# Optimization experiments

Hardware: AMD Instinct MI355X
Metric: run time of the kernel (lower is better)

Reference implementation:

```python
import jax, jax.numpy as jnp
import numpy as np

B, S, E, A, DK, H = 8, 2048, 256, 16, 64, 64  # batch, seq, embed, action, d_key, mlp hidden


def setup_inputs() -> dict:
    key = jax.random.key(0)
    ks = jax.random.split(key, 8)
    obs = jax.random.normal(ks[0], (B, S, E), dtype=jnp.float32)
    act = jnp.zeros((B, S, A), dtype=jnp.float32)  # one-hot actions; unused by forward
    # projection weights stored as [in, out] (torch Linear applies x @ W.T)
    Wq = jax.random.normal(ks[1], (E, DK), dtype=jnp.float32) / np.sqrt(E)
    Wk = jax.random.normal(ks[2], (E, DK), dtype=jnp.float32) / np.sqrt(E)
    Wv = jax.random.normal(ks[3], (E, DK), dtype=jnp.float32) / np.sqrt(E)
    W1 = jax.random.normal(ks[4], (DK, H), dtype=jnp.float32) / np.sqrt(DK)
    b1 = jnp.zeros((H,), dtype=jnp.float32)
    W2 = jax.random.normal(ks[5], (H, 1), dtype=jnp.float32) / np.sqrt(H)
    b2 = jnp.zeros((1,), dtype=jnp.float32)
    return dict(obs=obs, act=act, Wq=Wq, Wk=Wk, Wv=Wv, W1=W1, b1=b1, W2=W2, b2=b2)


def reference(obs, act, Wq, Wk, Wv, W1, b1, W2, b2):
    b, s, _ = obs.shape
    dk = Wq.shape[1]
    scale = dk ** -0.25  # applied to both q and k, net 1/sqrt(dk)
    q = (obs @ Wq) * scale          # [b, s, dk]
    k = (obs @ Wk) * scale          # [b, s, dk]
    v = obs @ Wv                    # [b, s, dk]
    scores = jnp.einsum('bqd,bkd->bqk', q, k)  # [b, s, s]
    causal = jnp.tril(jnp.ones((s, s), dtype=bool))
    scores = jnp.where(causal[None], scores, -jnp.inf)
    attn = jax.nn.softmax(scores, axis=2)      # [b, s, s]
    attn_out = jnp.einsum('bqk,bkd->bqd', attn, v)  # [b, s, dk]
    h = jax.nn.relu(attn_out.reshape(b * s, dk) @ W1 + b1)
    x = h @ W2 + b2                 # [b*s, 1]
    return (x, attn)
```

## Files before the change

### kernel.cpp

```cpp
#include <hip/hip_runtime.h>
#include <hip/hip_bf16.h>
#include <math.h>

#define NB 8
#define SQ 2048
#define NSP 8

typedef __attribute__((ext_vector_type(8))) short short8;
typedef __attribute__((ext_vector_type(4))) float f32x4;

__device__ __forceinline__ short f2bf(float f) {
    union { float f; unsigned u; } v; v.f = f;
    unsigned r = v.u + 0x7FFF + ((v.u >> 16) & 1);
    return (short)(r >> 16);
}
__device__ __forceinline__ float bf2f(short s) {
    union { unsigned u; float f; } v; v.u = ((unsigned)(unsigned short)s) << 16;
    return v.f;
}

__global__ __launch_bounds__(256) void k_wt(const float* __restrict__ Wq,
                                            const float* __restrict__ Wk,
                                            const float* __restrict__ Wv,
                                            short* __restrict__ wt) {
    int o = blockIdx.x * 256 + threadIdx.x;
    int row = o >> 8, e = o & 255;
    int w = row >> 6, d = row & 63;
    const float* W = (w == 0) ? Wq : ((w == 1) ? Wk : Wv);
    wt[o] = f2bf(W[e * 64 + d]);
}

__global__ __launch_bounds__(256, 4) void k_proj(const float* __restrict__ obs,
                                                 const short* __restrict__ wt,
                                                 short* __restrict__ qw,
                                                 short* __restrict__ kw,
                                                 short* __restrict__ vt) {
    int tid = threadIdx.x, w = tid >> 6, l = tid & 63, lg = l >> 4, lc = l & 15;
    int r0 = blockIdx.x * 16;
    int arow = r0 + lc;
    f32x4 accq = {0.f,0.f,0.f,0.f}, acck = {0.f,0.f,0.f,0.f}, accv = {0.f,0.f,0.f,0.f};
    const short* wq = wt + (size_t)(w * 16 + lc) * 256;
    const short* wk = wt + (size_t)(64 + w * 16 + lc) * 256;
    const short* wv = wt + (size_t)(128 + w * 16 + lc) * 256;
    #pragma unroll
    for (int ks = 0; ks < 8; ++ks) {
        int e0 = ks * 32 + lg * 8;
        const float* ap = obs + (size_t)arow * 256 + e0;
        float4 f0 = *(const float4*)ap;
        float4 f1 = *(const float4*)(ap + 4);
        short8 a;
        a[0] = f2bf(f0.x); a[1] = f2bf(f0.y); a[2] = f2bf(f0.z); a[3] = f2bf(f0.w);
        a[4] = f2bf(f1.x); a[5] = f2bf(f1.y); a[6] = f2bf(f1.z); a[7] = f2bf(f1.w);
        accq = __builtin_amdgcn_mfma_f32_16x16x32_bf16(a, *(const short8*)(wq + e0), accq, 0, 0, 0);
        acck = __builtin_amdgcn_mfma_f32_16x16x32_bf16(a, *(const short8*)(wk + e0), acck, 0, 0, 0);
        accv = __builtin_amdgcn_mfma_f32_16x16x32_bf16(a, *(const short8*)(wv + e0), accv, 0, 0, 0);
    }
    const float scale = 0.35355339059327373f;
    __shared__ short ldsv[64][18];
    #pragma unroll
    for (int r = 0; r < 4; ++r) {
        int row = r0 + lg * 4 + r;
        qw[(size_t)row * 64 + w * 16 + lc] = f2bf(accq[r] * scale);
        kw[(size_t)row * 64 + w * 16 + lc] = f2bf(acck[r] * scale);
        ldsv[w * 16 + lc][lg * 4 + r] = f2bf(accv[r]);
    }
    __syncthreads();
    int b = r0 >> 11, s0 = r0 & 2047;
    int d = tid >> 2, sc = (tid & 3) * 4;
    short* dst = vt + (size_t)b * 64 * SQ + (size_t)d * SQ + s0 + sc;
    dst[0] = ldsv[d][sc]; dst[1] = ldsv[d][sc + 1];
    dst[2] = ldsv[d][sc + 2]; dst[3] = ldsv[d][sc + 3];
}

__global__ __launch_bounds__(256) void k_flash(const short* __restrict__ qw,
                                               const short* __restrict__ kw,
                                               const short* __restrict__ vt,
                                               float* __restrict__ op,
                                               float* __restrict__ lpart,
                                               short* __restrict__ pbuf) {
    int qb = blockIdx.x, sp = blockIdx.y, b = blockIdx.z;
    if (sp > qb) return;
    int q0 = qb * 64;
    int tid = threadIdx.x, w = tid >> 6, l = tid & 63, lg = l >> 4, lc = l & 15;
    int r0 = q0 + w * 16;
    int eo = lg * 8;
    __shared__ short ldsP[4][16][72];
    const short* qbase = qw + (size_t)b * SQ * 64;
    const short* kbase = kw + (size_t)b * SQ * 64;
    const short* vbase = vt + (size_t)b * 64 * SQ;
    short* pbase = pbuf + (size_t)b * SQ * SQ;
    short8 qf0 = *(const short8*)(qbase + (size_t)(r0 + lc) * 64 + eo);
    short8 qf1 = *(const short8*)(qbase + (size_t)(r0 + lc) * 64 + 32 + eo);
    float lsum[4];
    f32x4 o[4];
    #pragma unroll
    for (int r = 0; r < 4; ++r) lsum[r] = 0.f;
    #pragma unroll
    for (int nj = 0; nj < 4; ++nj) o[nj] = (f32x4){0.f, 0.f, 0.f, 0.f};

    for (int kb = sp; kb <= qb; kb += NSP) {
        int k0 = kb * 64;
        f32x4 s[4];
        #pragma unroll
        for (int nj = 0; nj < 4; ++nj) s[nj] = (f32x4){0.f, 0.f, 0.f, 0.f};
        #pragma unroll
        for (int nj = 0; nj < 4; ++nj) {
            short8 kf = *(const short8*)(kbase + (size_t)(k0 + nj * 16 + lc) * 64 + eo);
            s[nj] = __builtin_amdgcn_mfma_f32_16x16x32_bf16(qf0, kf, s[nj], 0, 0, 0);
        }
        #pragma unroll
        for (int nj = 0; nj < 4; ++nj) {
            short8 kf = *(const short8*)(kbase + (size_t)(k0 + nj * 16 + lc) * 64 + 32 + eo);
            s[nj] = __builtin_amdgcn_mfma_f32_16x16x32_bf16(qf1, kf, s[nj], 0, 0, 0);
        }
        if (kb == qb) {
            #pragma unroll
            for (int nj = 0; nj < 4; ++nj)
                #pragma unroll
                for (int r = 0; r < 4; ++r)
                    if (k0 + nj * 16 + lc > r0 + lg * 4 + r) s[nj][r] = -INFINITY;
        }
        #pragma unroll
        for (int r = 0; r < 4; ++r) {
            float ps = 0.f;
            #pragma unroll
            for (int nj = 0; nj < 4; ++nj) {
                float p = __expf(s[nj][r]);
                ps += p;
                ldsP[w][lg * 4 + r][nj * 16 + lc] = f2bf(p);
            }
            ps += __shfl_xor(ps, 1);
            ps += __shfl_xor(ps, 2);
            ps += __shfl_xor(ps, 4);
            ps += __shfl_xor(ps, 8);
            lsum[r] += ps;
        }
        #pragma unroll
        for (int ks = 0; ks < 2; ++ks) {
            short8 pa = *(const short8*)&ldsP[w][lc][ks * 32 + lg * 8];
            *(short8*)(pbase + (size_t)(r0 + lc) * SQ + k0 + ks * 32 + lg * 8) = pa;
            #pragma unroll
            for (int nj = 0; nj < 4; ++nj) {
                short8 vf = *(const short8*)(vbase + (size_t)(nj * 16 + lc) * SQ + k0 + ks * 32 + eo);
                o[nj] = __builtin_amdgcn_mfma_f32_16x16x32_bf16(pa, vf, o[nj], 0, 0, 0);
            }
        }
    }
    size_t pb = ((size_t)sp * NB + b) * SQ;
    #pragma unroll
    for (int r = 0; r < 4; ++r) {
        int row = r0 + lg * 4 + r;
        if (lc == 0) lpart[pb + row] = lsum[r];
        #pragma unroll
        for (int nj = 0; nj < 4; ++nj)
            op[(pb + row) * 64 + nj * 16 + lc] = o[nj][r];
    }
}

__global__ __launch_bounds__(256) void k_combine(const float* __restrict__ op,
                                                 const float* __restrict__ lpart,
                                                 const float* __restrict__ W1,
                                                 const float* __restrict__ b1,
                                                 const float* __restrict__ W2,
                                                 const float* __restrict__ b2,
                                                 float* __restrict__ x,
                                                 float* __restrict__ linv) {
    int row0 = blockIdx.x * 8;
    int tid = threadIdx.x, w = tid >> 6, l = tid & 63;
    __shared__ float w1l[64][64];
    __shared__ float aol[8][64];
    {
        const float4* src = (const float4*)W1;
        float4* dst = (float4*)&w1l[0][0];
        #pragma unroll
        for (int i = 0; i < 4; ++i) dst[tid + i * 256] = src[tid + i * 256];
    }
    #pragma unroll
    for (int rr = 0; rr < 2; ++rr) {
        int grow = row0 + w * 2 + rr;
        int b = grow >> 11, s = grow & 2047;
        int nsp = (s >> 6) + 1; if (nsp > NSP) nsp = NSP;
        float od = 0.f, lt = 0.f;
        for (int sp = 0; sp < nsp; ++sp) {
            size_t base = (size_t)(sp * NB + b) * SQ + s;
            od += op[base * 64 + l];
            lt += lpart[base];
        }
        float inv = 1.f / lt;
        aol[w * 2 + rr][l] = od * inv;
        if (l == 0) linv[grow] = inv;
    }
    __syncthreads();
    #pragma unroll
    for (int rr = 0; rr < 2; ++rr) {
        int grow = row0 + w * 2 + rr;
        float t = b1[l];
        #pragma unroll 16
        for (int d = 0; d < 64; ++d) t += aol[w * 2 + rr][d] * w1l[d][l];
        float h = fmaxf(t, 0.f);
        float px = h * W2[l];
        px += __shfl_xor(px, 1);
        px += __shfl_xor(px, 2);
        px += __shfl_xor(px, 4);
        px += __shfl_xor(px, 8);
        px += __shfl_xor(px, 16);
        px += __shfl_xor(px, 32);
        if (l == 0) x[grow] = px + b2[0];
    }
}

__global__ __launch_bounds__(256) void k_write(const short* __restrict__ pbuf,
                                               const float* __restrict__ linv,
                                               float* __restrict__ attn) {
    int csp = blockIdx.x, qb = blockIdx.y, b = blockIdx.z;
    int tid = threadIdx.x, w = tid >> 6, l = tid & 63;
    __shared__ float liv[64];
    if (tid < 64) liv[tid] = linv[(size_t)b * SQ + qb * 64 + tid];
    __syncthreads();
    float* abase = attn + (size_t)b * SQ * SQ;
    int colb = csp * 256 + l * 4;
    if ((colb >> 6) > qb) {
        float4 z = {0.f, 0.f, 0.f, 0.f};
        #pragma unroll
        for (int r = 0; r < 16; ++r) {
            int row = qb * 64 + w * 16 + r;
            *(float4*)(abase + (size_t)row * SQ + colb) = z;
        }
        return;
    }
    const short* pbase = pbuf + (size_t)b * SQ * SQ;
    #pragma unroll
    for (int r = 0; r < 16; ++r) {
        int row = qb * 64 + w * 16 + r;
        float inv = liv[w * 16 + r];
        short4 pv = *(const short4*)(pbase + (size_t)row * SQ + colb);
        float4 o;
        o.x = bf2f(pv.x) * inv;
        o.y = bf2f(pv.y) * inv;
        o.z = bf2f(pv.z) * inv;
        o.w = bf2f(pv.w) * inv;
        *(float4*)(abase + (size_t)row * SQ + colb) = o;
    }
}

extern "C" void kernel_launch(void* const* d_in, const int* in_sizes, int n_in,
                              void* d_out, int out_size, void* d_ws, size_t ws_size,
                              hipStream_t stream) {
    const float* obs = (const float*)d_in[0];
    const float* Wq  = (const float*)d_in[2];
    const float* Wk  = (const float*)d_in[3];
    const float* Wv  = (const float*)d_in[4];
    const float* W1  = (const float*)d_in[5];
    const float* b1  = (const float*)d_in[6];
    const float* W2  = (const float*)d_in[7];
    const float* b2  = (const float*)d_in[8];

    float* x    = (float*)d_out;
    float* attn = (float*)d_out + NB * SQ;

    float* op = attn;

    char* ws = (char*)d_ws;
    short* wt    = (short*)(ws);
    short* qw    = (short*)(ws + 131072);
    short* kw    = (short*)(ws + 2228224);
    short* vt    = (short*)(ws + 4325376);
    float* lpart = (float*)(ws + 6422528);
    float* linv  = (float*)(ws + 6946816);
    short* pbuf  = (short*)(ws + 7012352);

    k_wt<<<dim3(192), dim3(256), 0, stream>>>(Wq, Wk, Wv, wt);
    k_proj<<<dim3(1024), dim3(256), 0, stream>>>(obs, wt, qw, kw, vt);
    k_flash<<<dim3(32, NSP, NB), dim3(256), 0, stream>>>(qw, kw, vt, op, lpart, pbuf);
    k_combine<<<dim3(2048), dim3(256), 0, stream>>>(op, lpart, W1, b1, W2, b2, x, linv);
    k_write<<<dim3(8, 32, NB), dim3(256), 0, stream>>>(pbuf, linv, attn);
}
```

Baseline: 143.0 us.

## Fuse all stages into one cooperative persistent kernel with grid syncs

Replaces the five separate launches (weight transpose, projection, flash attention, combine, attn write) with a single cooperative persistent kernel. Each stage loops over work items by block index and is separated from the next by grid.sync(), so per-launch gaps and tail effects are removed. The row-sum of softmax probabilities is now taken with an MFMA against a vector of bf16 ones instead of shuffle reductions, which sums the bf16-rounded values rather than the fp32 ones. Grid barriers and the smaller grid size (set from occupancy) may cost load balance compared with separate launches, and the original launch path is kept as a fallback.

Measured after the change: 355.3 us. 148% more time.

```diff
diff --git a/kernel.cpp b/kernel.cpp
--- a/kernel.cpp
+++ b/kernel.cpp
@@ -1,5 +1,6 @@
 #include <hip/hip_runtime.h>
 #include <hip/hip_bf16.h>
+#include <hip/hip_cooperative_groups.h>
 #include <math.h>
 
 #define NB 8
@@ -17,6 +18,226 @@
 __device__ __forceinline__ float bf2f(short s) {
     union { unsigned u; float f; } v; v.u = ((unsigned)(unsigned short)s) << 16;
     return v.f;
+}
+
+__global__ __launch_bounds__(256, 4) void k_mega(
+    const float* __restrict__ obs, const float* __restrict__ Wq,
+    const float* __restrict__ Wk,  const float* __restrict__ Wv,
+    const float* __restrict__ W1,  const float* __restrict__ b1,
+    const float* __restrict__ W2,  const float* __restrict__ b2,
+    float* __restrict__ x, float* __restrict__ attn,
+    short* __restrict__ wt, short* __restrict__ qw, short* __restrict__ kw,
+    short* __restrict__ vt, float* __restrict__ lpart, float* __restrict__ linv,
+    short* __restrict__ pbuf, float* __restrict__ op)
+{
+    namespace cg = cooperative_groups;
+    cg::grid_group grid = cg::this_grid();
+    __shared__ __align__(16) char smem[18688];
+    const int bid = threadIdx.y * 0 + blockIdx.x;
+    const int tid = threadIdx.x, w = tid >> 6, l = tid & 63, lg = l >> 4, lc = l & 15;
+    const int gsz = gridDim.x;
+    short8 ones;
+    #pragma unroll
+    for (int i = 0; i < 8; ++i) ones[i] = (short)0x3F80;
+
+    for (int o = bid * 256 + tid; o < 192 * 256; o += gsz * 256) {
+        int row = o >> 8, e = o & 255;
+        int wsel = row >> 6, d = row & 63;
+        const float* W = (wsel == 0) ? Wq : ((wsel == 1) ? Wk : Wv);
+        wt[o] = f2bf(W[e * 64 + d]);
+    }
+    grid.sync();
+
+    {
+        short (*ldsv)[18] = (short(*)[18])smem;
+        for (int tb = bid; tb < 1024; tb += gsz) {
+            int r0 = tb * 16;
+            int arow = r0 + lc;
+            f32x4 accq = {0.f,0.f,0.f,0.f}, acck = {0.f,0.f,0.f,0.f}, accv = {0.f,0.f,0.f,0.f};
+            const short* wqp = wt + (size_t)(w * 16 + lc) * 256;
+            const short* wkp = wt + (size_t)(64 + w * 16 + lc) * 256;
+            const short* wvp = wt + (size_t)(128 + w * 16 + lc) * 256;
+            #pragma unroll
+            for (int ks = 0; ks < 8; ++ks) {
+                int e0 = ks * 32 + lg * 8;
+                const float* ap = obs + (size_t)arow * 256 + e0;
+                float4 f0 = *(const float4*)ap;
+                float4 f1 = *(const float4*)(ap + 4);
+                short8 a;
+                a[0] = f2bf(f0.x); a[1] = f2bf(f0.y); a[2] = f2bf(f0.z); a[3] = f2bf(f0.w);
+                a[4] = f2bf(f1.x); a[5] = f2bf(f1.y); a[6] = f2bf(f1.z); a[7] = f2bf(f1.w);
+                accq = __builtin_amdgcn_mfma_f32_16x16x32_bf16(a, *(const short8*)(wqp + e0), accq, 0, 0, 0);
+                acck = __builtin_amdgcn_mfma_f32_16x16x32_bf16(a, *(const short8*)(wkp + e0), acck, 0, 0, 0);
+                accv = __builtin_amdgcn_mfma_f32_16x16x32_bf16(a, *(const short8*)(wvp + e0), accv, 0, 0, 0);
+            }
+            const float scale = 0.35355339059327373f;
+            #pragma unroll
+            for (int r = 0; r < 4; ++r) {
+                int row = r0 + lg * 4 + r;
+                qw[(size_t)row * 64 + w * 16 + lc] = f2bf(accq[r] * scale);
+                kw[(size_t)row * 64 + w * 16 + lc] = f2bf(acck[r] * scale);
+                ldsv[w * 16 + lc][lg * 4 + r] = f2bf(accv[r]);
+            }
+            __syncthreads();
+            int b = r0 >> 11, s0 = r0 & 2047;
+            int d = tid >> 2, sc = (tid & 3) * 4;
+            short* dst = vt + (size_t)b * 64 * SQ + (size_t)d * SQ + s0 + sc;
+            dst[0] = ldsv[d][sc]; dst[1] = ldsv[d][sc + 1];
+            dst[2] = ldsv[d][sc + 2]; dst[3] = ldsv[d][sc + 3];
+            __syncthreads();
+        }
+    }
+    grid.sync();
+
+    {
+        short (*ldsP)[16][72] = (short(*)[16][72])smem;
+        for (int vb = bid; vb < 32 * NSP * NB; vb += gsz) {
+            int qb = vb & 31, sp = (vb >> 5) & 7, b = vb >> 8;
+            if (sp > qb) continue;
+            int q0 = qb * 64;
+            int r0 = q0 + w * 16;
+            int eo = lg * 8;
+            const short* qbase = qw + (size_t)b * SQ * 64;
+            const short* kbase = kw + (size_t)b * SQ * 64;
+            const short* vbase = vt + (size_t)b * 64 * SQ;
+            short* pbase = pbuf + (size_t)b * SQ * SQ;
+            short8 qf0 = *(const short8*)(qbase + (size_t)(r0 + lc) * 64 + eo);
+            short8 qf1 = *(const short8*)(qbase + (size_t)(r0 + lc) * 64 + 32 + eo);
+            f32x4 osum = {0.f, 0.f, 0.f, 0.f};
+            f32x4 o[4];
+            #pragma unroll
+            for (int nj = 0; nj < 4; ++nj) o[nj] = (f32x4){0.f, 0.f, 0.f, 0.f};
+
+            for (int kb = sp; kb <= qb; kb += NSP) {
+                int k0 = kb * 64;
+                f32x4 s[4];
+                #pragma unroll
+                for (int nj = 0; nj < 4; ++nj) s[nj] = (f32x4){0.f, 0.f, 0.f, 0.f};
+                #pragma unroll
+                for (int nj = 0; nj < 4; ++nj) {
+                    short8 kf = *(const short8*)(kbase + (size_t)(k0 + nj * 16 + lc) * 64 + eo);
+                    s[nj] = __builtin_amdgcn_mfma_f32_16x16x32_bf16(qf0, kf, s[nj], 0, 0, 0);
+                }
+                #pragma unroll
+                for (int nj = 0; nj < 4; ++nj) {
+                    short8 kf = *(const short8*)(kbase + (size_t)(k0 + nj * 16 + lc) * 64 + 32 + eo);
+                    s[nj] = __builtin_amdgcn_mfma_f32_16x16x32_bf16(qf1, kf, s[nj], 0, 0, 0);
+                }
+                if (kb == qb) {
+                    #pragma unroll
+                    for (int nj = 0; nj < 4; ++nj)
+                        #pragma unroll
+                        for (int r = 0; r < 4; ++r)
+                            if (k0 + nj * 16 + lc > r0 + lg * 4 + r) s[nj][r] = -INFINITY;
+                }
+                #pragma unroll
+                for (int r = 0; r < 4; ++r)
+                    #pragma unroll
+                    for (int nj = 0; nj < 4; ++nj)
+                        ldsP[w][lg * 4 + r][nj * 16 + lc] = f2bf(__expf(s[nj][r]));
+                #pragma unroll
+                for (int ks = 0; ks < 2; ++ks) {
+                    short8 pa = *(const short8*)&ldsP[w][lc][ks * 32 + lg * 8];
+                    *(short8*)(pbase + (size_t)(r0 + lc) * SQ + k0 + ks * 32 + lg * 8) = pa;
+                    osum = __builtin_amdgcn_mfma_f32_16x16x32_bf16(pa, ones, osum, 0, 0, 0);
+                    #pragma unroll
+                    for (int nj = 0; nj < 4; ++nj) {
+                        short8 vf = *(const short8*)(vbase + (size_t)(nj * 16 + lc) * SQ + k0 + ks * 32 + eo);
+                        o[nj] = __builtin_amdgcn_mfma_f32_16x16x32_bf16(pa, vf, o[nj], 0, 0, 0);
+                    }
+                }
+            }
+            size_t pb = ((size_t)sp * NB + b) * SQ;
+            #pragma unroll
+            for (int r = 0; r < 4; ++r) {
+                int row = r0 + lg * 4 + r;
+                if (lc == 0) lpart[pb + row] = osum[r];
+                #pragma unroll
+                for (int nj = 0; nj < 4; ++nj)
+                    op[(pb + row) * 64 + nj * 16 + lc] = o[nj][r];
+            }
+        }
+    }
+    grid.sync();
+
+    {
+        float* w1l = (float*)smem;
+        float (*aol)[64] = (float(*)[64])(smem + 16384);
+        const float4* src = (const float4*)W1;
+        float4* dst = (float4*)w1l;
+        #pragma unroll
+        for (int i = 0; i < 4; ++i) dst[tid + i * 256] = src[tid + i * 256];
+        __syncthreads();
+        for (int vb = bid; vb < 2048; vb += gsz) {
+            int row0 = vb * 8;
+            #pragma unroll
+            for (int rr = 0; rr < 2; ++rr) {
+                int grow = row0 + w * 2 + rr;
+                int b = grow >> 11, s = grow & 2047;
+                int nsp = (s >> 6) + 1; if (nsp > NSP) nsp = NSP;
+                float od = 0.f, lt = 0.f;
+                for (int sp = 0; sp < nsp; ++sp) {
+                    size_t base = (size_t)(sp * NB + b) * SQ + s;
+                    od += op[base * 64 + l];
+                    lt += lpart[base];
+                }
+                float inv = 1.f / lt;
+                aol[w * 2 + rr][l] = od * inv;
+                if (l == 0) linv[grow] = inv;
+            }
+            #pragma unroll
+            for (int rr = 0; rr < 2; ++rr) {
+                int grow = row0 + w * 2 + rr;
+                float t = b1[l];
+                #pragma unroll 16
+                for (int d = 0; d < 64; ++d) t += aol[w * 2 + rr][d] * w1l[d * 64 + l];
+                float h = fmaxf(t, 0.f);
+                float px = h * W2[l];
+                px += __shfl_xor(px, 1);
+                px += __shfl_xor(px, 2);
+                px += __shfl_xor(px, 4);
+                px += __shfl_xor(px, 8);
+                px += __shfl_xor(px, 16);
+                px += __shfl_xor(px, 32);
+                if (l == 0) x[grow] = px + b2[0];
+            }
+        }
+    }
+    grid.sync();
+
+    {
+        float* liv = (float*)smem;
+        for (int vb = bid; vb < 2048; vb += gsz) {
+            int csp = vb & 7, qb = (vb >> 3) & 31, b = vb >> 8;
+            __syncthreads();
+            if (tid < 64) liv[tid] = linv[(size_t)b * SQ + qb * 64 + tid];
+            __syncthreads();
+            float* abase = attn + (size_t)b * SQ * SQ;
+            int colb = csp * 256 + l * 4;
+            if ((colb >> 6) > qb) {
+                float4 z = {0.f, 0.f, 0.f, 0.f};
+                #pragma unroll
+                for (int r = 0; r < 16; ++r) {
+                    int row = qb * 64 + w * 16 + r;
+                    *(float4*)(abase + (size_t)row * SQ + colb) = z;
+                }
+            } else {
+                const short* pbase = pbuf + (size_t)b * SQ * SQ;
+                #pragma unroll
+                for (int r = 0; r < 16; ++r) {
+                    int row = qb * 64 + w * 16 + r;
+                    float inv = liv[w * 16 + r];
+                    short4 pv = *(const short4*)(pbase + (size_t)row * SQ + colb);
+                    float4 o;
+                    o.x = bf2f(pv.x) * inv;
+                    o.y = bf2f(pv.y) * inv;
+                    o.z = bf2f(pv.z) * inv;
+                    o.w = bf2f(pv.w) * inv;
+                    *(float4*)(abase + (size_t)row * SQ + colb) = o;
+                }
+            }
+        }
+    }
 }
 
 __global__ __launch_bounds__(256) void k_wt(const float* __restrict__ Wq,
@@ -91,10 +312,11 @@
     short* pbase = pbuf + (size_t)b * SQ * SQ;
     short8 qf0 = *(const short8*)(qbase + (size_t)(r0 + lc) * 64 + eo);
     short8 qf1 = *(const short8*)(qbase + (size_t)(r0 + lc) * 64 + 32 + eo);
-    float lsum[4];
+    short8 ones;
+    #pragma unroll
+    for (int i = 0; i < 8; ++i) ones[i] = (short)0x3F80;
+    f32x4 osum = {0.f, 0.f, 0.f, 0.f};
     f32x4 o[4];
-    #pragma unroll
-    for (int r = 0; r < 4; ++r) lsum[r] = 0.f;
     #pragma unroll
     for (int nj = 0; nj < 4; ++nj) o[nj] = (f32x4){0.f, 0.f, 0.f, 0.f};
 
@@ -121,24 +343,15 @@
                     if (k0 + nj * 16 + lc > r0 + lg * 4 + r) s[nj][r] = -INFINITY;
         }
         #pragma unroll
-        for (int r = 0; r < 4; ++r) {
-            float ps = 0.f;
-            #pragma unroll
-            for (int nj = 0; nj < 4; ++nj) {
-                float p = __expf(s[nj][r]);
-                ps += p;
-                ldsP[w][lg * 4 + r][nj * 16 + lc] = f2bf(p);
-            }
-            ps += __shfl_xor(ps, 1);
-            ps += __shfl_xor(ps, 2);
-            ps += __shfl_xor(ps, 4);
-            ps += __shfl_xor(ps, 8);
-            lsum[r] += ps;
-        }
+        for (int r = 0; r < 4; ++r)
+            #pragma unroll
+            for (int nj = 0; nj < 4; ++nj)
+                ldsP[w][lg * 4 + r][nj * 16 + lc] = f2bf(__expf(s[nj][r]));
         #pragma unroll
         for (int ks = 0; ks < 2; ++ks) {
             short8 pa = *(const short8*)&ldsP[w][lc][ks * 32 + lg * 8];
             *(short8*)(pbase + (size_t)(r0 + lc) * SQ + k0 + ks * 32 + lg * 8) = pa;
+            osum = __builtin_amdgcn_mfma_f32_16x16x32_bf16(pa, ones, osum, 0, 0, 0);
             #pragma unroll
             for (int nj = 0; nj < 4; ++nj) {
                 short8 vf = *(const short8*)(vbase + (size_t)(nj * 16 + lc) * SQ + k0 + ks * 32 + eo);
@@ -150,7 +363,7 @@
     #pragma unroll
     for (int r = 0; r < 4; ++r) {
         int row = r0 + lg * 4 + r;
-        if (lc == 0) lpart[pb + row] = lsum[r];
+        if (lc == 0) lpart[pb + row] = osum[r];
         #pragma unroll
         for (int nj = 0; nj < 4; ++nj)
             op[(pb + row) * 64 + nj * 16 + lc] = o[nj][r];
@@ -257,8 +470,7 @@
 
     float* x    = (float*)d_out;
     float* attn = (float*)d_out + NB * SQ;
-
-    float* op = attn;
+    float* op   = attn;
 
     char* ws = (char*)d_ws;
     short* wt    = (short*)(ws);
@@ -269,9 +481,26 @@
     float* linv  = (float*)(ws + 6946816);
     short* pbuf  = (short*)(ws + 7012352);
 
-    k_wt<<<dim3(192), dim3(256), 0, stream>>>(Wq, Wk, Wv, wt);
-    k_proj<<<dim3(1024), dim3(256), 0, stream>>>(obs, wt, qw, kw, vt);
-    k_flash<<<dim3(32, NSP, NB), dim3(256), 0, stream>>>(qw, kw, vt, op, lpart, pbuf);
-    k_combine<<<dim3(2048), dim3(256), 0, stream>>>(op, lpart, W1, b1, W2, b2, x, linv);
-    k_write<<<dim3(8, 32, NB), dim3(256), 0, stream>>>(pbuf, linv, attn);
-}
+    int maxb = 0;
+    hipError_t qrc = hipOccupancyMaxActiveBlocksPerMultiprocessor(&maxb, k_mega, 256, 0);
+    if (qrc != hipSuccess || maxb < 1) maxb = 2;
+    int grid = 256 * maxb;
+    if (grid > 1024) grid = 1024;
+
+    void* args[] = {&obs, &Wq, &Wk, &Wv, &W1, &b1, &W2, &b2, &x, &attn,
+                    &wt, &qw, &kw, &vt, &lpart, &linv, &pbuf, &op};
+    hipError_t rc = hipLaunchCooperativeKernel((void*)k_mega, dim3(grid), dim3(256),
+                                               args, 0, stream);
+    if (rc != hipSuccess && grid > 512) {
+        grid = 512;
+        rc = hipLaunchCooperativeKernel((void*)k_mega, dim3(grid), dim3(256),
+                                        args, 0, stream);
+    }
+    if (rc != hipSuccess) {
+        k_wt<<<dim3(192), dim3(256), 0, stream>>>(Wq, Wk, Wv, wt);
+        k_proj<<<dim3(1024), dim3(256), 0, stream>>>(obs, wt, qw, kw, vt);
+        k_flash<<<dim3(32, NSP, NB), dim3(256), 0, stream>>>(qw, kw, vt, op, lpart, pbuf);
+        k_combine<<<dim3(2048), dim3(256), 0, stream>>>(op, lpart, W1, b1, W2, b2, x, linv);
+        k_write<<<dim3(8, 32, NB), dim3(256), 0, stream>>>(pbuf, linv, attn);
+    }
+}
```
